# Kernel optimization log

Hardware: AMD Instinct MI355X
Metric: run time of the kernel (lower is better)

## Reference

```python
import jax, jax.numpy as jnp
import numpy as np

N = 50000
LEAKY_SLOPE = 0.2


def gat_layer(x, src, dst, W, a_src, a_dst, bias, concat):
    """PyG-style GATConv (eval mode, self-loops already in src/dst).
    x: [N, Fin]; W: [Fin, H*C]; a_src, a_dst: [H, C]; bias: [H*C] or [C].
    """
    H, C = a_src.shape
    h = (x @ W).reshape(-1, H, C)                      # [N, H, C]
    alpha_src = jnp.einsum('nhc,hc->nh', h, a_src)      # [N, H]
    alpha_dst = jnp.einsum('nhc,hc->nh', h, a_dst)      # [N, H]
    e = jax.nn.leaky_relu(alpha_src[src] + alpha_dst[dst], LEAKY_SLOPE)  # [E, H]
    # scatter-softmax over incoming edges of each destination node
    m = jax.lax.stop_gradient(jax.ops.segment_max(e, dst, num_segments=N))
    e = jnp.exp(e - m[dst])
    denom = jax.ops.segment_sum(e, dst, num_segments=N)  # [N, H]
    alpha = e / (denom[dst] + 1e-16)                     # [E, H]
    msg = h[src] * alpha[:, :, None]                     # [E, H, C]
    out = jax.ops.segment_sum(msg, dst, num_segments=N)  # [N, H, C]
    out = out.reshape(-1, H * C) if concat else out.mean(axis=1)
    return out + bias


def setup_inputs() -> dict:
    key = jax.random.key(0)
    ks = jax.random.split(key, 10)
    Fin, Hd, Hh = 256, 64, 4
    E = 1600000
    x = jax.random.normal(ks[0], (N, Fin), dtype=jnp.float32)
    edge_index = jax.random.randint(ks[1], (2, E), 0, N, dtype=jnp.int64)
    s = 1.0 / np.sqrt(Fin)
    W1 = jax.random.normal(ks[2], (Fin, Hh * Hd), dtype=jnp.float32) * s
    att_src1 = jax.random.normal(ks[3], (Hh, Hd), dtype=jnp.float32) * (1.0 / np.sqrt(Hd))
    att_dst1 = jax.random.normal(ks[4], (Hh, Hd), dtype=jnp.float32) * (1.0 / np.sqrt(Hd))
    b1 = jnp.zeros((Hh * Hd,), dtype=jnp.float32)
    W2 = jax.random.normal(ks[5], (Hh * Hd, Hd), dtype=jnp.float32) * (1.0 / np.sqrt(Hh * Hd))
    att_src2 = jax.random.normal(ks[6], (1, Hd), dtype=jnp.float32) * (1.0 / np.sqrt(Hd))
    att_dst2 = jax.random.normal(ks[7], (1, Hd), dtype=jnp.float32) * (1.0 / np.sqrt(Hd))
    b2 = jnp.zeros((Hd,), dtype=jnp.float32)
    return {"x": x, "edge_index": edge_index, "W1": W1, "att_src1": att_src1,
            "att_dst1": att_dst1, "b1": b1, "W2": W2, "att_src2": att_src2,
            "att_dst2": att_dst2, "b2": b2}


def reference(x, edge_index, W1, att_src1, att_dst1, b1, W2, att_src2, att_dst2, b2):
    # PyG GATConv adds self-loops by default
    loop = jnp.arange(N, dtype=edge_index.dtype)
    src = jnp.concatenate([edge_index[0], loop])
    dst = jnp.concatenate([edge_index[1], loop])
    h = gat_layer(x, src, dst, W1, att_src1, att_dst1, b1, concat=True)
    h = jax.nn.elu(h)            # dropout is identity in eval mode
    out = gat_layer(h, src, dst, W2, att_src2, att_dst2, b2, concat=False)
    return out
```

## Files before the change

kernel.cpp:

```cpp
#include <hip/hip_runtime.h>


typedef __attribute__((ext_vector_type(8))) short short8;
typedef __attribute__((ext_vector_type(4))) float floatx4;

#define FIN 256
#define H1 4
#define CH 64
#define CAP 16384

__device__ __forceinline__ float bf2f(ushort u) {
    union { unsigned int i; float f; } v; v.i = ((unsigned int)u) << 16; return v.f;
}
__device__ __forceinline__ ushort f2bf(float f) {
    union { float f; unsigned int i; } v; v.f = f;
    unsigned int r = v.i + 0x7fffu + ((v.i >> 16) & 1u);
    return (ushort)(r >> 16);
}
__device__ __forceinline__ float load_in(const void* p, int i, int f) {
    return f ? ((const float*)p)[i] : bf2f(((const ushort*)p)[i]);
}
__device__ __forceinline__ int load_idx(const void* p, long long i, int f64) {
    return f64 ? (int)((const long long*)p)[i] : ((const int*)p)[i];
}

__global__ __launch_bounds__(256) void probe_kernel(const ushort* __restrict__ x,
                                                    const int* __restrict__ ei,
                                                    int* __restrict__ flags,
                                                    int* __restrict__ bcnt) {
    __shared__ int s_nan, s_odd;
    int t = threadIdx.x;
    bcnt[t] = 0;
    if (t == 0) { s_nan = 0; s_odd = 0; }
    __syncthreads();
    int nanc = 0, oddc = 0;
    for (int i = t; i < 16384; i += 256) {
        ushort u = x[i];
        if (((u >> 7) & 0xFF) == 0xFF) nanc++;
    }
    for (int i = t; i < 2048; i += 256)
        if (ei[2 * i + 1] != 0) oddc++;
    if (nanc) atomicAdd(&s_nan, nanc);
    if (oddc) atomicAdd(&s_odd, oddc);
    __syncthreads();
    if (t == 0) {
        flags[0] = (s_nan >= 2) ? 1 : 0;
        flags[1] = (s_odd == 0) ? 1 : 0;
    }
}

__global__ __launch_bounds__(256) void prep_bucket_kernel(
        const void* __restrict__ x, const void* __restrict__ W1,
        const void* __restrict__ W2, ushort* __restrict__ xb,
        ushort* __restrict__ Wt1, ushort* __restrict__ Wt2,
        const void* __restrict__ ei, int* __restrict__ bcnt,
        unsigned int* __restrict__ buckets,
        int E, int Etot, int Nn, const int* __restrict__ flags,
        int PB_conv, int PB_tr_end) {
    __shared__ int lcnt[256], lbase[256], lcur[256];
    int bid = blockIdx.x, t = threadIdx.x;
    int f = flags[0];
    if (bid < PB_conv) {
        int i0 = bid * 2048 + t * 8;
        if (f) {
            float4 v0 = ((const float4*)x)[i0 / 4];
            float4 v1 = ((const float4*)x)[i0 / 4 + 1];
            ushort4 o0, o1;
            o0.x = f2bf(v0.x); o0.y = f2bf(v0.y); o0.z = f2bf(v0.z); o0.w = f2bf(v0.w);
            o1.x = f2bf(v1.x); o1.y = f2bf(v1.y); o1.z = f2bf(v1.z); o1.w = f2bf(v1.w);
            *(ushort4*)(xb + i0) = o0;
            *(ushort4*)(xb + i0 + 4) = o1;
        } else {
            *(uint4*)(xb + i0) = ((const uint4*)x)[i0 / 8];
        }
        return;
    }
    if (bid < PB_tr_end) {
        int j = (bid - PB_conv) * 256 + t;
        if (j < FIN * FIN) {
            int n = j / FIN, k = j % FIN;
            Wt1[j] = f2bf(load_in(W1, k * FIN + n, f));
        } else {
            int jj = j - FIN * FIN;
            int n = jj / FIN, k = jj % FIN;
            Wt2[jj] = f2bf(load_in(W2, k * CH + n, f));
        }
        return;
    }
    lcnt[t] = 0; lcur[t] = 0;
    __syncthreads();
    int f64 = flags[1];
    int base = (bid - PB_tr_end) * 4096 + t;
    unsigned int val[16]; int bk[16]; bool ok[16];
#pragma unroll
    for (int j = 0; j < 16; ++j) {
        int e = base + j * 256;
        ok[j] = e < Etot;
        bk[j] = 0; val[j] = 0;
        if (ok[j]) {
            int s, d;
// ... 93 lines not shown
                    alphaD[row * H + head] = pd;
                }
#pragma unroll
                for (int nt = 0; nt < 4; nt++) {
                    int col = cbase + nt * 16 + l16;
                    size_t caddr = planar
                        ? ((size_t)(col >> 7) * M + row) * 128 + (col & 127)
                        : (size_t)row * Nc + col;
                    C[caddr] = f2bf(acc[mt][nt][r]);
                }
            }
        }
    }
}

__global__ __launch_bounds__(256) void gemm1_pass2_kernel(
        const ushort* __restrict__ A, const ushort* __restrict__ Bt,
        ushort* __restrict__ C, int M, int K, int Nc,
        const void* __restrict__ aS, const void* __restrict__ aD,
        float* __restrict__ alphaS, float* __restrict__ alphaD,
        const int* __restrict__ flags, int g1, int nbx,
        const int* __restrict__ bcnt, const unsigned int* __restrict__ buckets,
        int* __restrict__ offs, int* __restrict__ csr_src, int Nn) {
    __shared__ int part[256], sc[256], cur[256];
    int bid = blockIdx.x;
    int t = threadIdx.x;
    if (bid < g1) {
        gemm_core(A, Bt, C, M, K, Nc, aS, aD, alphaS, alphaD, 4, flags[0],
                  bid % nbx, bid / nbx, 1);
        return;
    }
    int b = bid - g1;
    part[t] = bcnt[t];
    __syncthreads();
#pragma unroll
    for (int off = 1; off < 256; off <<= 1) {
        int v = (t >= off) ? part[t - off] : 0;
        __syncthreads();
        part[t] += v;
        __syncthreads();
    }
    int basepos = (b == 0) ? 0 : part[b - 1];
    int nEdges = min(bcnt[b], CAP);
    sc[t] = 0;
    __syncthreads();
    const unsigned int* bk = buckets + (size_t)b * CAP;
    for (int i = t; i < nEdges; i += 256)
        atomicAdd(&sc[bk[i] & 255], 1);
    __syncthreads();
    int mycount = sc[t];
    __syncthreads();
#pragma unroll
    for (int off = 1; off < 256; off <<= 1) {
        int v = (t >= off) ? sc[t - off] : 0;
        __syncthreads();
        sc[t] += v;
        __syncthreads();
    }
    int excl = sc[t] - mycount;
    int gnode = b * 256 + t;
    if (gnode <= Nn) offs[gnode] = basepos + excl;
    cur[t] = excl;
    __syncthreads();
    for (int i = t; i < nEdges; i += 256) {
        unsigned int v = bk[i];
        int p = atomicAdd(&cur[v & 255], 1);
        csr_src[basepos + p] = (int)(v >> 8);
    }
}

__global__ __launch_bounds__(256) void gemm2_kernel(const ushort* __restrict__ A,
                                                    const ushort* __restrict__ Bt,
                                                    ushort* __restrict__ C,
                                                    int M, int K, int Nc,
                                                    const void* __restrict__ aS,
                                                    const void* __restrict__ aD,
                                                    float* __restrict__ alphaS,
                                                    float* __restrict__ alphaD,
                                                    const int* __restrict__ flags) {
    gemm_core(A, Bt, C, M, K, Nc, aS, aD, alphaS, alphaD, 1, flags[0],
              blockIdx.x, blockIdx.y, 0);
}

__global__ __launch_bounds__(256) void gat_node1_pass(
        const int* __restrict__ csr_src, const int* __restrict__ offs,
        const float* __restrict__ asrc, const float* __restrict__ adst,
        const ushort* __restrict__ h1p, const void* __restrict__ b1,
        ushort* __restrict__ hmidb, int Nn, const int* __restrict__ flags,
        int plane) {
    int f = flags[0];
    int wave = threadIdx.x >> 6, lane = threadIdx.x & 63;
    int n = blockIdx.x * 4 + wave;
    if (n >= Nn) return;
    int half = lane >> 5, l5 = lane & 31;
    int head = plane * 2 + (l5 >> 4);
    float ad = adst[n * H1 + head];
    unsigned rowoff = (unsigned)(plane * Nn) * 128u + (unsigned)l5 * 4u;
    int beg = offs[n], end = offs[n + 1];
    float a0 = 0.f, a1 = 0.f, a2 = 0.f, a3 = 0.f, l = 0.f;

    int e = beg;
    while (e + 16 <= end) {
        int sj[8]; float aj[8]; uint2 vj[8];
#pragma unroll
        for (int j = 0; j < 8; ++j) sj[j] = csr_src[e + 2 * j + half];
#pragma unroll
        for (int j = 0; j < 8; ++j) {
            aj[j] = asrc[sj[j] * H1 + head];
            vj[j] = *(const uint2*)(h1p + rowoff + (unsigned)sj[j] * 128u);
        }
#pragma unroll
        for (int j = 0; j < 8; ++j) {
            float s = aj[j] + ad;
            s = fmaxf(s, 0.2f * s);
            float p = __expf(s);
            l += p;
            union { unsigned int i; float fl; } c0, c1, c2, c3;
            c0.i = vj[j].x << 16; c1.i = vj[j].x & 0xffff0000u;
            c2.i = vj[j].y << 16; c3.i = vj[j].y & 0xffff0000u;
            a0 += p * c0.fl; a1 += p * c1.fl;
            a2 += p * c2.fl; a3 += p * c3.fl;
        }
        e += 16;
    }
    if (e < end) {
        int sj[8]; float aj[8]; uint2 vj[8];
#pragma unroll
        for (int j = 0; j < 8; ++j) {
            int ei = e + 2 * j + half;
            sj[j] = csr_src[ei < end ? ei : beg];
        }
#pragma unroll
        for (int j = 0; j < 8; ++j) {
            int ei = e + 2 * j + half;
            aj[j] = (ei < end) ? asrc[sj[j] * H1 + head] : -1e30f;
            vj[j] = *(const uint2*)(h1p + rowoff + (unsigned)sj[j] * 128u);
        }
#pragma unroll
        for (int j = 0; j < 8; ++j) {
            float s = aj[j] + ad;
            s = fmaxf(s, 0.2f * s);
            float p = __expf(s);
            l += p;
            union { unsigned int i; float fl; } c0, c1, c2, c3;
            c0.i = vj[j].x << 16; c1.i = vj[j].x & 0xffff0000u;
            c2.i = vj[j].y << 16; c3.i = vj[j].y & 0xffff0000u;
            a0 += p * c0.fl; a1 += p * c1.fl;
            a2 += p * c2.fl; a3 += p * c3.fl;
        }
    }
    a0 += __shfl_xor(a0, 32); a1 += __shfl_xor(a1, 32);
    a2 += __shfl_xor(a2, 32); a3 += __shfl_xor(a3, 32);
    l  += __shfl_xor(l, 32);
    if (half == 0) {
        float inv = 1.f / (l + 1e-16f);
        int cb = plane * 128 + l5 * 4;
        float o0 = a0 * inv + load_in(b1, cb + 0, f);
        float o1 = a1 * inv + load_in(b1, cb + 1, f);
        float o2 = a2 * inv + load_in(b1, cb + 2, f);
        float o3 = a3 * inv + load_in(b1, cb + 3, f);
        o0 = o0 > 0.f ? o0 : __expf(o0) - 1.f;
        o1 = o1 > 0.f ? o1 : __expf(o1) - 1.f;
        o2 = o2 > 0.f ? o2 : __expf(o2) - 1.f;
        o3 = o3 > 0.f ? o3 : __expf(o3) - 1.f;
        uint2 st;
        st.x = (unsigned int)f2bf(o0) | ((unsigned int)f2bf(o1) << 16);
        st.y = (unsigned int)f2bf(o2) | ((unsigned int)f2bf(o3) << 16);
        *(uint2*)(hmidb + (unsigned)n * 256u + (unsigned)cb) = st;
    }
}

__global__ __launch_bounds__(256) void gat_node2(const int* __restrict__ csr_src,
                                                 const int* __restrict__ offs,
                                                 const float* __restrict__ asrc,
                                                 const float* __restrict__ adst,
                                                 const ushort* __restrict__ h2b,
                                                 const void* __restrict__ b2,
                                                 void* __restrict__ out, int Nn,
                                                 const int* __restrict__ flags) {
    int f = flags[0];
    int wave = threadIdx.x >> 6, lane = threadIdx.x & 63;
    int n = blockIdx.x * 4 + wave;
    if (n >= Nn) return;
    int q = lane >> 4, l4 = lane & 15;
    float ad = adst[n];
    int beg = offs[n], end = offs[n + 1];
    float a0 = 0.f, a1 = 0.f, a2 = 0.f, a3 = 0.f, l = 0.f;

    int e = beg;
    while (e + 16 <= end) {
        int sj[4]; float aj[4]; uint2 vj[4];
#pragma unroll
        for (int j = 0; j < 4; ++j) sj[j] = csr_src[e + 4 * j + q];
#pragma unroll
        for (int j = 0; j < 4; ++j) {
            aj[j] = asrc[sj[j]];
            vj[j] = *(const uint2*)(h2b + (unsigned)sj[j] * 64u + (unsigned)l4 * 4u);
        }
#pragma unroll
        for (int j = 0; j < 4; ++j) {
            float s = aj[j] + ad;
            s = fmaxf(s, 0.2f * s);
            float p = __expf(s);
            l += p;
            union { unsigned int i; float fl; } c0, c1, c2, c3;
            c0.i = vj[j].x << 16; c1.i = vj[j].x & 0xffff0000u;
            c2.i = vj[j].y << 16; c3.i = vj[j].y & 0xffff0000u;
            a0 += p * c0.fl; a1 += p * c1.fl;
            a2 += p * c2.fl; a3 += p * c3.fl;
        }
        e += 16;
    }
    if (e < end) {
        int sj[4]; float aj[4]; uint2 vj[4];
#pragma unroll
        for (int j = 0; j < 4; ++j) {
            int ei = e + 4 * j + q;
            sj[j] = csr_src[ei < end ? ei : beg];
        }
#pragma unroll
        for (int j = 0; j < 4; ++j) {
            int ei = e + 4 * j + q;
            aj[j] = (ei < end) ? asrc[sj[j]] : -1e30f;
            vj[j] = *(const uint2*)(h2b + (unsigned)sj[j] * 64u + (unsigned)l4 * 4u);
        }
#pragma unroll
        for (int j = 0; j < 4; ++j) {
            float s = aj[j] + ad;
            s = fmaxf(s, 0.2f * s);
            float p = __expf(s);
            l += p;
            union { unsigned int i; float fl; } c0, c1, c2, c3;
            c0.i = vj[j].x << 16; c1.i = vj[j].x & 0xffff0000u;
            c2.i = vj[j].y << 16; c3.i = vj[j].y & 0xffff0000u;
            a0 += p * c0.fl; a1 += p * c1.fl;
            a2 += p * c2.fl; a3 += p * c3.fl;
        }
    }
#pragma unroll
    for (int off = 16; off <= 32; off <<= 1) {
        a0 += __shfl_xor(a0, off); a1 += __shfl_xor(a1, off);
        a2 += __shfl_xor(a2, off); a3 += __shfl_xor(a3, off);
        l  += __shfl_xor(l, off);
    }
    if (lane < 16) {
        float inv = 1.f / (l + 1e-16f);
        float o0 = a0 * inv + load_in(b2, l4 * 4 + 0, f);
        float o1 = a1 * inv + load_in(b2, l4 * 4 + 1, f);
        float o2 = a2 * inv + load_in(b2, l4 * 4 + 2, f);
        float o3 = a3 * inv + load_in(b2, l4 * 4 + 3, f);
        if (f) {
            float4 st; st.x = o0; st.y = o1; st.z = o2; st.w = o3;
            *(float4*)((float*)out + (unsigned)n * 64u + (unsigned)l4 * 4u) = st;
        } else {
            uint2 st;
            st.x = (unsigned int)f2bf(o0) | ((unsigned int)f2bf(o1) << 16);
            st.y = (unsigned int)f2bf(o2) | ((unsigned int)f2bf(o3) << 16);
            *(uint2*)((ushort*)out + (unsigned)n * 64u + (unsigned)l4 * 4u) = st;
        }
    }
}

extern "C" void kernel_launch(void* const* d_in, const int* in_sizes, int n_in,
                              void* d_out, int out_size, void* d_ws, size_t ws_size,
                              hipStream_t stream) {
    const void* x   = d_in[0];
    const void* ei  = d_in[1];
    const void* W1  = d_in[2];
    const void* as1 = d_in[3];
    const void* ad1 = d_in[4];
    const void* b1  = d_in[5];
    const void* W2  = d_in[6];
    const void* as2 = d_in[7];
    const void* ad2 = d_in[8];
    const void* b2  = d_in[9];

    const int Nn = in_sizes[0] / FIN;
    const int E  = in_sizes[1] / 2;
    const int ET = E + Nn;
    const int NB = (Nn + 255) >> 8;

    char* ws = (char*)d_ws;
    size_t off = 0;
    auto alloc = [&](size_t bytes) {
        size_t o = off;
        off += (bytes + 255) & ~(size_t)255;
        return o;
    };
    ushort* xb    = (ushort*)(ws + alloc((size_t)Nn * FIN * 2));
    ushort* h1b   = (ushort*)(ws + alloc((size_t)Nn * FIN * 2));
    ushort* hmidb = (ushort*)(ws + alloc((size_t)Nn * FIN * 2));
    ushort* h2b   = (ushort*)(ws + alloc((size_t)Nn * CH * 2));
    ushort* Wt1   = (ushort*)(ws + alloc((size_t)FIN * FIN * 2));
    ushort* Wt2   = (ushort*)(ws + alloc((size_t)CH * FIN * 2));
    float* as1f   = (float*)(ws + alloc((size_t)Nn * H1 * 4));
    float* ad1f   = (float*)(ws + alloc((size_t)Nn * H1 * 4));
    float* as2f   = (float*)(ws + alloc((size_t)Nn * 4));
    float* ad2f   = (float*)(ws + alloc((size_t)Nn * 4));
    int*   offs   = (int*)(ws + alloc((size_t)(Nn + 1) * 4));
    int*   csr    = (int*)(ws + alloc((size_t)ET * 4));
    unsigned int* buckets = (unsigned int*)(ws + alloc((size_t)256 * CAP * 4));
    int*   bcnt   = (int*)(ws + alloc(256 * 4));
    int*   flags  = (int*)(ws + alloc(256));
    (void)ws_size; (void)n_in; (void)out_size;

    probe_kernel<<<1, 256, 0, stream>>>((const ushort*)x, (const int*)ei, flags, bcnt);

    int PB_conv = (Nn * FIN) / 2048;
    int PB_tr   = (FIN * FIN + CH * FIN) / 256;
    int PB_bkt  = (ET + 4095) / 4096;
    prep_bucket_kernel<<<PB_conv + PB_tr + PB_bkt, 256, 0, stream>>>(
        x, W1, W2, xb, Wt1, Wt2, ei, bcnt, buckets,
        E, ET, Nn, flags, PB_conv, PB_conv + PB_tr);

    int nbx = (Nn + 255) / 256;
    int g1 = nbx * H1;
    gemm1_pass2_kernel<<<g1 + NB, 256, 0, stream>>>(
        xb, Wt1, h1b, Nn, FIN, FIN, as1, ad1, as1f, ad1f,
        flags, g1, nbx, bcnt, buckets, offs, csr, Nn);

    gat_node1_pass<<<(Nn + 3) / 4, 256, 0, stream>>>(
        csr, offs, as1f, ad1f, h1b, b1, hmidb, Nn, flags, 0);
    gat_node1_pass<<<(Nn + 3) / 4, 256, 0, stream>>>(
        csr, offs, as1f, ad1f, h1b, b1, hmidb, Nn, flags, 1);

    gemm2_kernel<<<dim3((Nn + 255) / 256, 1), 256, 0, stream>>>(
        hmidb, Wt2, h2b, Nn, FIN, CH, as2, ad2, as2f, ad2f, flags);
    gat_node2<<<(Nn + 3) / 4, 256, 0, stream>>>(csr, offs, as2f, ad2f, h2b, b2, d_out, Nn, flags);
}
```

Before: 362.3 us.

## Precompute packed per-edge attention weights before aggregation passes

Two new per-node kernels compute the per-edge exp attention weights and the per-node inverse softmax denominators once per layer. They store each weight in bf16, packed together with the source index: two uint2 arrays for the layer-1 head pairs, and a single 32-bit word per edge for layer 2. The aggregation kernels then read these packed records instead of gathering asrc, recomputing leaky-relu and exp, and reducing the denominator, and the layer-1 aggregation switches to 16-byte feature loads with 8 channels per lane. This removes redundant attention math and gathers from the bandwidth-bound aggregation loops. In exchange it adds two extra edge passes and extra workspace traffic, rounds attention weights to bf16, and assumes node indices fit in 16 bits for layer 2.

```diff
diff --git a/kernel.cpp b/kernel.cpp
--- a/kernel.cpp
+++ b/kernel.cpp
@@ -16,6 +16,9 @@
     union { float f; unsigned int i; } v; v.f = f;
     unsigned int r = v.i + 0x7fffu + ((v.i >> 16) & 1u);
     return (ushort)(r >> 16);
+}
+__device__ __forceinline__ float bits2f(unsigned int b) {
+    union { unsigned int i; float f; } v; v.i = b; return v.f;
 }
 __device__ __forceinline__ float load_in(const void* p, int i, int f) {
     return f ? ((const float*)p)[i] : bf2f(((const ushort*)p)[i]);
@@ -275,98 +278,171 @@
               blockIdx.x, blockIdx.y, 0);
 }
 
+__global__ __launch_bounds__(256) void wk1_kernel(const int* __restrict__ csr_src,
+                                                  const int* __restrict__ offs,
+                                                  const float* __restrict__ asrc,
+                                                  const float* __restrict__ adst,
+                                                  uint2* __restrict__ pkA,
+                                                  uint2* __restrict__ pkB,
+                                                  float* __restrict__ invl, int Nn) {
+    int wave = threadIdx.x >> 6, lane = threadIdx.x & 63;
+    int n = blockIdx.x * 4 + wave;
+    if (n >= Nn) return;
+    float4 ad = *(const float4*)(adst + (size_t)n * 4);
+    int beg = offs[n], end = offs[n + 1];
+    float l0 = 0.f, l1 = 0.f, l2 = 0.f, l3 = 0.f;
+    for (int e0 = beg; e0 < end; e0 += 64) {
+        int e = e0 + lane;
+        bool v = e < end;
+        int src = v ? csr_src[e] : 0;
+        float4 as = *(const float4*)(asrc + (size_t)src * 4);
+        float s0 = as.x + ad.x, s1 = as.y + ad.y, s2 = as.z + ad.z, s3 = as.w + ad.w;
+        s0 = fmaxf(s0, 0.2f * s0); s1 = fmaxf(s1, 0.2f * s1);
+        s2 = fmaxf(s2, 0.2f * s2); s3 = fmaxf(s3, 0.2f * s3);
+        float p0 = v ? __expf(s0) : 0.f, p1 = v ? __expf(s1) : 0.f;
+        float p2 = v ? __expf(s2) : 0.f, p3 = v ? __expf(s3) : 0.f;
+        l0 += p0; l1 += p1; l2 += p2; l3 += p3;
+        if (v) {
+            uint2 a, b;
+            a.x = (unsigned int)src;
+            a.y = (unsigned int)f2bf(p0) | ((unsigned int)f2bf(p1) << 16);
+            b.x = (unsigned int)src;
+            b.y = (unsigned int)f2bf(p2) | ((unsigned int)f2bf(p3) << 16);
+            pkA[e] = a; pkB[e] = b;
+        }
+    }
+#pragma unroll
+    for (int off = 1; off < 64; off <<= 1) {
+        l0 += __shfl_xor(l0, off); l1 += __shfl_xor(l1, off);
+        l2 += __shfl_xor(l2, off); l3 += __shfl_xor(l3, off);
+    }
+    if (lane == 0) {
+        float4 iv;
+        iv.x = 1.f / (l0 + 1e-16f); iv.y = 1.f / (l1 + 1e-16f);
+        iv.z = 1.f / (l2 + 1e-16f); iv.w = 1.f / (l3 + 1e-16f);
+        *(float4*)(invl + (size_t)n * 4) = iv;
+    }
+}
+
+__global__ __launch_bounds__(256) void wk2_kernel(const int* __restrict__ csr_src,
+                                                  const int* __restrict__ offs,
+                                                  const float* __restrict__ asrc,
+                                                  const float* __restrict__ adst,
+                                                  unsigned int* __restrict__ pk2,
+                                                  float* __restrict__ invl2, int Nn) {
+    int wave = threadIdx.x >> 6, lane = threadIdx.x & 63;
+    int n = blockIdx.x * 4 + wave;
+    if (n >= Nn) return;
+    float ad = adst[n];
+    int beg = offs[n], end = offs[n + 1];
+    float l = 0.f;
+    for (int e0 = beg; e0 < end; e0 += 64) {
+        int e = e0 + lane;
+        bool v = e < end;
+        int src = v ? csr_src[e] : 0;
+        float s = asrc[src] + ad;
+        s = fmaxf(s, 0.2f * s);
+        float p = v ? __expf(s) : 0.f;
+        l += p;
+        if (v) pk2[e] = (unsigned int)src | ((unsigned int)f2bf(p) << 16);
+    }
+#pragma unroll
+    for (int off = 1; off < 64; off <<= 1) l += __shfl_xor(l, off);
+    if (lane == 0) invl2[n] = 1.f / (l + 1e-16f);
+}
+
 __global__ __launch_bounds__(256) void gat_node1_pass(
-        const int* __restrict__ csr_src, const int* __restrict__ offs,
-        const float* __restrict__ asrc, const float* __restrict__ adst,
-        const ushort* __restrict__ h1p, const void* __restrict__ b1,
-        ushort* __restrict__ hmidb, int Nn, const int* __restrict__ flags,
-        int plane) {
+        const uint2* __restrict__ pk, const int* __restrict__ offs,
+        const float* __restrict__ invl, const ushort* __restrict__ h1p,
+        const void* __restrict__ b1, ushort* __restrict__ hmidb,
+        int Nn, const int* __restrict__ flags, int plane) {
     int f = flags[0];
     int wave = threadIdx.x >> 6, lane = threadIdx.x & 63;
     int n = blockIdx.x * 4 + wave;
     if (n >= Nn) return;
-    int half = lane >> 5, l5 = lane & 31;
-    int head = plane * 2 + (l5 >> 4);
-    float ad = adst[n * H1 + head];
-    unsigned rowoff = (unsigned)(plane * Nn) * 128u + (unsigned)l5 * 4u;
+    int g = lane >> 4, l4 = lane & 15;
+    bool hi = l4 >= 8;
+    const ushort* base = h1p + (size_t)plane * Nn * 128 + (size_t)l4 * 8;
     int beg = offs[n], end = offs[n + 1];
-    float a0 = 0.f, a1 = 0.f, a2 = 0.f, a3 = 0.f, l = 0.f;
+    float a0 = 0.f, a1 = 0.f, a2 = 0.f, a3 = 0.f;
+    float a4 = 0.f, a5 = 0.f, a6 = 0.f, a7 = 0.f;
 
     int e = beg;
-    while (e + 16 <= end) {
-        int sj[8]; float aj[8]; uint2 vj[8];
-#pragma unroll
-        for (int j = 0; j < 8; ++j) sj[j] = csr_src[e + 2 * j + half];
-#pragma unroll
-        for (int j = 0; j < 8; ++j) {
-            aj[j] = asrc[sj[j] * H1 + head];
-            vj[j] = *(const uint2*)(h1p + rowoff + (unsigned)sj[j] * 128u);
-        }
-#pragma unroll
-        for (int j = 0; j < 8; ++j) {
-            float s = aj[j] + ad;
-            s = fmaxf(s, 0.2f * s);
-            float p = __expf(s);
-            l += p;
-            union { unsigned int i; float fl; } c0, c1, c2, c3;
-            c0.i = vj[j].x << 16; c1.i = vj[j].x & 0xffff0000u;
-            c2.i = vj[j].y << 16; c3.i = vj[j].y & 0xffff0000u;
-            a0 += p * c0.fl; a1 += p * c1.fl;
-            a2 += p * c2.fl; a3 += p * c3.fl;
-        }
-        e += 16;
+    while (e + 8 <= end) {
+        uint2 k0 = pk[e + g];
+        uint2 k1 = pk[e + 4 + g];
+        uint4 v0 = *(const uint4*)(base + (size_t)k0.x * 128);
+        uint4 v1 = *(const uint4*)(base + (size_t)k1.x * 128);
+        float p0 = bits2f(hi ? (k0.y & 0xffff0000u) : (k0.y << 16));
+        float p1 = bits2f(hi ? (k1.y & 0xffff0000u) : (k1.y << 16));
+        a0 += p0 * bits2f(v0.x << 16); a1 += p0 * bits2f(v0.x & 0xffff0000u);
+        a2 += p0 * bits2f(v0.y << 16); a3 += p0 * bits2f(v0.y & 0xffff0000u);
+        a4 += p0 * bits2f(v0.z << 16); a5 += p0 * bits2f(v0.z & 0xffff0000u);
+        a6 += p0 * bits2f(v0.w << 16); a7 += p0 * bits2f(v0.w & 0xffff0000u);
+        a0 += p1 * bits2f(v1.x << 16); a1 += p1 * bits2f(v1.x & 0xffff0000u);
+        a2 += p1 * bits2f(v1.y << 16); a3 += p1 * bits2f(v1.y & 0xffff0000u);
+        a4 += p1 * bits2f(v1.z << 16); a5 += p1 * bits2f(v1.z & 0xffff0000u);
+        a6 += p1 * bits2f(v1.w << 16); a7 += p1 * bits2f(v1.w & 0xffff0000u);
+        e += 8;
     }
     if (e < end) {
-        int sj[8]; float aj[8]; uint2 vj[8];
-#pragma unroll
-        for (int j = 0; j < 8; ++j) {
-            int ei = e + 2 * j + half;
-            sj[j] = csr_src[ei < end ? ei : beg];
-        }
-#pragma unroll
-        for (int j = 0; j < 8; ++j) {
-            int ei = e + 2 * j + half;
-            aj[j] = (ei < end) ? asrc[sj[j] * H1 + head] : -1e30f;
-            vj[j] = *(const uint2*)(h1p + rowoff + (unsigned)sj[j] * 128u);
-        }
-#pragma unroll
-        for (int j = 0; j < 8; ++j) {
-            float s = aj[j] + ad;
-            s = fmaxf(s, 0.2f * s);
-            float p = __expf(s);
-            l += p;
-            union { unsigned int i; float fl; } c0, c1, c2, c3;
-            c0.i = vj[j].x << 16; c1.i = vj[j].x & 0xffff0000u;
-            c2.i = vj[j].y << 16; c3.i = vj[j].y & 0xffff0000u;
-            a0 += p * c0.fl; a1 += p * c1.fl;
-            a2 += p * c2.fl; a3 += p * c3.fl;
-        }
-    }
-    a0 += __shfl_xor(a0, 32); a1 += __shfl_xor(a1, 32);
-    a2 += __shfl_xor(a2, 32); a3 += __shfl_xor(a3, 32);
-    l  += __shfl_xor(l, 32);
-    if (half == 0) {
-        float inv = 1.f / (l + 1e-16f);
-        int cb = plane * 128 + l5 * 4;
+        int i0 = e + g, i1 = e + 4 + g;
+        uint2 k0, k1;
+        k0.x = 0u; k0.y = 0u; k1.x = 0u; k1.y = 0u;
+        if (i0 < end) k0 = pk[i0];
+        if (i1 < end) k1 = pk[i1];
+        uint4 v0 = *(const uint4*)(base + (size_t)k0.x * 128);
+        uint4 v1 = *(const uint4*)(base + (size_t)k1.x * 128);
+        float p0 = bits2f(hi ? (k0.y & 0xffff0000u) : (k0.y << 16));
+        float p1 = bits2f(hi ? (k1.y & 0xffff0000u) : (k1.y << 16));
+        a0 += p0 * bits2f(v0.x << 16); a1 += p0 * bits2f(v0.x & 0xffff0000u);
+        a2 += p0 * bits2f(v0.y << 16); a3 += p0 * bits2f(v0.y & 0xffff0000u);
+        a4 += p0 * bits2f(v0.z << 16); a5 += p0 * bits2f(v0.z & 0xffff0000u);
+        a6 += p0 * bits2f(v0.w << 16); a7 += p0 * bits2f(v0.w & 0xffff0000u);
+        a0 += p1 * bits2f(v1.x << 16); a1 += p1 * bits2f(v1.x & 0xffff0000u);
+        a2 += p1 * bits2f(v1.y << 16); a3 += p1 * bits2f(v1.y & 0xffff0000u);
+        a4 += p1 * bits2f(v1.z << 16); a5 += p1 * bits2f(v1.z & 0xffff0000u);
+        a6 += p1 * bits2f(v1.w << 16); a7 += p1 * bits2f(v1.w & 0xffff0000u);
+    }
+#pragma unroll
+    for (int off = 16; off <= 32; off <<= 1) {
+        a0 += __shfl_xor(a0, off); a1 += __shfl_xor(a1, off);
+        a2 += __shfl_xor(a2, off); a3 += __shfl_xor(a3, off);
+        a4 += __shfl_xor(a4, off); a5 += __shfl_xor(a5, off);
+        a6 += __shfl_xor(a6, off); a7 += __shfl_xor(a7, off);
+    }
+    if (lane < 16) {
+        int head = plane * 2 + (l4 >> 3);
+        float inv = invl[(size_t)n * 4 + head];
+        int cb = plane * 128 + l4 * 8;
         float o0 = a0 * inv + load_in(b1, cb + 0, f);
         float o1 = a1 * inv + load_in(b1, cb + 1, f);
         float o2 = a2 * inv + load_in(b1, cb + 2, f);
         float o3 = a3 * inv + load_in(b1, cb + 3, f);
+        float o4 = a4 * inv + load_in(b1, cb + 4, f);
+        float o5 = a5 * inv + load_in(b1, cb + 5, f);
+        float o6 = a6 * inv + load_in(b1, cb + 6, f);
+        float o7 = a7 * inv + load_in(b1, cb + 7, f);
         o0 = o0 > 0.f ? o0 : __expf(o0) - 1.f;
         o1 = o1 > 0.f ? o1 : __expf(o1) - 1.f;
         o2 = o2 > 0.f ? o2 : __expf(o2) - 1.f;
         o3 = o3 > 0.f ? o3 : __expf(o3) - 1.f;
-        uint2 st;
+        o4 = o4 > 0.f ? o4 : __expf(o4) - 1.f;
+        o5 = o5 > 0.f ? o5 : __expf(o5) - 1.f;
+        o6 = o6 > 0.f ? o6 : __expf(o6) - 1.f;
+        o7 = o7 > 0.f ? o7 : __expf(o7) - 1.f;
+        uint4 st;
         st.x = (unsigned int)f2bf(o0) | ((unsigned int)f2bf(o1) << 16);
         st.y = (unsigned int)f2bf(o2) | ((unsigned int)f2bf(o3) << 16);
-        *(uint2*)(hmidb + (unsigned)n * 256u + (unsigned)cb) = st;
-    }
-}
-
-__global__ __launch_bounds__(256) void gat_node2(const int* __restrict__ csr_src,
+        st.z = (unsigned int)f2bf(o4) | ((unsigned int)f2bf(o5) << 16);
+        st.w = (unsigned int)f2bf(o6) | ((unsigned int)f2bf(o7) << 16);
+        *(uint4*)(hmidb + (size_t)n * 256 + cb) = st;
+    }
+}
+
+__global__ __launch_bounds__(256) void gat_node2(const unsigned int* __restrict__ pk2,
                                                  const int* __restrict__ offs,
-                                                 const float* __restrict__ asrc,
-                                                 const float* __restrict__ adst,
+                                                 const float* __restrict__ invl2,
                                                  const ushort* __restrict__ h2b,
                                                  const void* __restrict__ b2,
                                                  void* __restrict__ out, int Nn,
@@ -375,81 +451,57 @@
     int wave = threadIdx.x >> 6, lane = threadIdx.x & 63;
     int n = blockIdx.x * 4 + wave;
     if (n >= Nn) return;
-    int q = lane >> 4, l4 = lane & 15;
-    float ad = adst[n];
+    int g = lane >> 4, l4 = lane & 15;
+    const ushort* base = h2b + (size_t)l4 * 4;
     int beg = offs[n], end = offs[n + 1];
-    float a0 = 0.f, a1 = 0.f, a2 = 0.f, a3 = 0.f, l = 0.f;
+    float a0 = 0.f, a1 = 0.f, a2 = 0.f, a3 = 0.f;
 
     int e = beg;
-    while (e + 16 <= end) {
-        int sj[4]; float aj[4]; uint2 vj[4];
-#pragma unroll
-        for (int j = 0; j < 4; ++j) sj[j] = csr_src[e + 4 * j + q];
-#pragma unroll
-        for (int j = 0; j < 4; ++j) {
-            aj[j] = asrc[sj[j]];
-            vj[j] = *(const uint2*)(h2b + (unsigned)sj[j] * 64u + (unsigned)l4 * 4u);
-        }
-#pragma unroll
-        for (int j = 0; j < 4; ++j) {
-            float s = aj[j] + ad;
-            s = fmaxf(s, 0.2f * s);
-            float p = __expf(s);
-            l += p;
-            union { unsigned int i; float fl; } c0, c1, c2, c3;
-            c0.i = vj[j].x << 16; c1.i = vj[j].x & 0xffff0000u;
-            c2.i = vj[j].y << 16; c3.i = vj[j].y & 0xffff0000u;
-            a0 += p * c0.fl; a1 += p * c1.fl;
-            a2 += p * c2.fl; a3 += p * c3.fl;
-        }
-        e += 16;
+    while (e + 8 <= end) {
+        unsigned int k0 = pk2[e + g];
+        unsigned int k1 = pk2[e + 4 + g];
+        uint2 v0 = *(const uint2*)(base + (size_t)(k0 & 0xffffu) * 64);
+        uint2 v1 = *(const uint2*)(base + (size_t)(k1 & 0xffffu) * 64);
+        float p0 = bits2f(k0 & 0xffff0000u);
+        float p1 = bits2f(k1 & 0xffff0000u);
+        a0 += p0 * bits2f(v0.x << 16); a1 += p0 * bits2f(v0.x & 0xffff0000u);
+        a2 += p0 * bits2f(v0.y << 16); a3 += p0 * bits2f(v0.y & 0xffff0000u);
+        a0 += p1 * bits2f(v1.x << 16); a1 += p1 * bits2f(v1.x & 0xffff0000u);
+        a2 += p1 * bits2f(v1.y << 16); a3 += p1 * bits2f(v1.y & 0xffff0000u);
+        e += 8;
     }
     if (e < end) {
-        int sj[4]; float aj[4]; uint2 vj[4];
-#pragma unroll
-        for (int j = 0; j < 4; ++j) {
-            int ei = e + 4 * j + q;
-            sj[j] = csr_src[ei < end ? ei : beg];
-        }
-#pragma unroll
-        for (int j = 0; j < 4; ++j) {
-            int ei = e + 4 * j + q;
-            aj[j] = (ei < end) ? asrc[sj[j]] : -1e30f;
-            vj[j] = *(const uint2*)(h2b + (unsigned)sj[j] * 64u + (unsigned)l4 * 4u);
-        }
-#pragma unroll
-        for (int j = 0; j < 4; ++j) {
-            float s = aj[j] + ad;
-            s = fmaxf(s, 0.2f * s);
-            float p = __expf(s);
-            l += p;
-            union { unsigned int i; float fl; } c0, c1, c2, c3;
-            c0.i = vj[j].x << 16; c1.i = vj[j].x & 0xffff0000u;
-            c2.i = vj[j].y << 16; c3.i = vj[j].y & 0xffff0000u;
-            a0 += p * c0.fl; a1 += p * c1.fl;
-            a2 += p * c2.fl; a3 += p * c3.fl;
-        }
+        int i0 = e + g, i1 = e + 4 + g;
+        unsigned int k0 = (i0 < end) ? pk2[i0] : 0u;
+        unsigned int k1 = (i1 < end) ? pk2[i1] : 0u;
+        uint2 v0 = *(const uint2*)(base + (size_t)(k0 & 0xffffu) * 64);
+        uint2 v1 = *(const uint2*)(base + (size_t)(k1 & 0xffffu) * 64);
+        float p0 = bits2f(k0 & 0xffff0000u);
+        float p1 = bits2f(k1 & 0xffff0000u);
+        a0 += p0 * bits2f(v0.x << 16); a1 += p0 * bits2f(v0.x & 0xffff0000u);
+        a2 += p0 * bits2f(v0.y << 16); a3 += p0 * bits2f(v0.y & 0xffff0000u);
+        a0 += p1 * bits2f(v1.x << 16); a1 += p1 * bits2f(v1.x & 0xffff0000u);
+        a2 += p1 * bits2f(v1.y << 16); a3 += p1 * bits2f(v1.y & 0xffff0000u);
     }
 #pragma unroll
     for (int off = 16; off <= 32; off <<= 1) {
         a0 += __shfl_xor(a0, off); a1 += __shfl_xor(a1, off);
         a2 += __shfl_xor(a2, off); a3 += __shfl_xor(a3, off);
-        l  += __shfl_xor(l, off);
     }
     if (lane < 16) {
-        float inv = 1.f / (l + 1e-16f);
+        float inv = invl2[n];
         float o0 = a0 * inv + load_in(b2, l4 * 4 + 0, f);
         float o1 = a1 * inv + load_in(b2, l4 * 4 + 1, f);
         float o2 = a2 * inv + load_in(b2, l4 * 4 + 2, f);
         float o3 = a3 * inv + load_in(b2, l4 * 4 + 3, f);
         if (f) {
             float4 st; st.x = o0; st.y = o1; st.z = o2; st.w = o3;
-            *(float4*)((float*)out + (unsigned)n * 64u + (unsigned)l4 * 4u) = st;
+            *(float4*)((float*)out + (size_t)n * 64 + l4 * 4) = st;
         } else {
             uint2 st;
             st.x = (unsigned int)f2bf(o0) | ((unsigned int)f2bf(o1) << 16);
             st.y = (unsigned int)f2bf(o2) | ((unsigned int)f2bf(o3) << 16);
-            *(uint2*)((ushort*)out + (unsigned)n * 64u + (unsigned)l4 * 4u) = st;
+            *(uint2*)((ushort*)out + (size_t)n * 64 + l4 * 4) = st;
         }
     }
 }
@@ -490,8 +542,13 @@
     float* ad1f   = (float*)(ws + alloc((size_t)Nn * H1 * 4));
     float* as2f   = (float*)(ws + alloc((size_t)Nn * 4));
     float* ad2f   = (float*)(ws + alloc((size_t)Nn * 4));
+    float* invl   = (float*)(ws + alloc((size_t)Nn * H1 * 4));
+    float* invl2  = (float*)(ws + alloc((size_t)Nn * 4));
     int*   offs   = (int*)(ws + alloc((size_t)(Nn + 1) * 4));
     int*   csr    = (int*)(ws + alloc((size_t)ET * 4));
+    uint2* pkA    = (uint2*)(ws + alloc((size_t)ET * 8));
+    uint2* pkB    = (uint2*)(ws + alloc((size_t)ET * 8));
+    unsigned int* pk2 = (unsigned int*)(ws + alloc((size_t)ET * 4));
     unsigned int* buckets = (unsigned int*)(ws + alloc((size_t)256 * CAP * 4));
     int*   bcnt   = (int*)(ws + alloc(256 * 4));
     int*   flags  = (int*)(ws + alloc(256));
@@ -512,12 +569,14 @@
         xb, Wt1, h1b, Nn, FIN, FIN, as1, ad1, as1f, ad1f,
         flags, g1, nbx, bcnt, buckets, offs, csr, Nn);
 
+    wk1_kernel<<<(Nn + 3) / 4, 256, 0, stream>>>(csr, offs, as1f, ad1f, pkA, pkB, invl, Nn);
     gat_node1_pass<<<(Nn + 3) / 4, 256, 0, stream>>>(
-        csr, offs, as1f, ad1f, h1b, b1, hmidb, Nn, flags, 0);
+        pkA, offs, invl, h1b, b1, hmidb, Nn, flags, 0);
     gat_node1_pass<<<(Nn + 3) / 4, 256, 0, stream>>>(
-        csr, offs, as1f, ad1f, h1b, b1, hmidb, Nn, flags, 1);
+        pkB, offs, invl, h1b, b1, hmidb, Nn, flags, 1);
 
     gemm2_kernel<<<dim3((Nn + 255) / 256, 1), 256, 0, stream>>>(
         hmidb, Wt2, h2b, Nn, FIN, CH, as2, ad2, as2f, ad2f, flags);
-    gat_node2<<<(Nn + 3) / 4, 256, 0, stream>>>(csr, offs, as2f, ad2f, h2b, b2, d_out, Nn, flags);
-}
+    wk2_kernel<<<(Nn + 3) / 4, 256, 0, stream>>>(csr, offs, as2f, ad2f, pk2, invl2, Nn);
+    gat_node2<<<(Nn + 3) / 4, 256, 0, stream>>>(pk2, offs, invl2, h2b, b2, d_out, Nn, flags);
+}
```

Measured after the change: 397.2 us. 1.1x slower.

## Split layer-1 aggregation: compute all-head weights once, reuse packed weights in second pass

Applied to the files above, without the earlier changes.

The first aggregation pass now computes softmax numerators for all four heads at once and writes each edge's source index plus its bf16 weights for heads 2-3 into a packed per-edge buffer, along with per-node inverse denominators. The second pass reads these packed entries instead of the CSR plus asrc gather and exp, so it only gathers feature rows. Both passes now use 16-byte feature loads, with 16 lanes covering a 128-wide plane and 4 edge groups per wave. This adds an 8-byte-per-edge write and read, and stores the head 2-3 weights in bf16, which reduces their precision.

```diff
diff --git a/kernel.cpp b/kernel.cpp
--- a/kernel.cpp
+++ b/kernel.cpp
@@ -16,6 +16,9 @@
     union { float f; unsigned int i; } v; v.f = f;
     unsigned int r = v.i + 0x7fffu + ((v.i >> 16) & 1u);
     return (ushort)(r >> 16);
+}
+__device__ __forceinline__ float bits2f(unsigned int b) {
+    union { unsigned int i; float f; } v; v.i = b; return v.f;
 }
 __device__ __forceinline__ float load_in(const void* p, int i, int f) {
     return f ? ((const float*)p)[i] : bf2f(((const ushort*)p)[i]);
@@ -275,91 +278,217 @@
               blockIdx.x, blockIdx.y, 0);
 }
 
-__global__ __launch_bounds__(256) void gat_node1_pass(
+__global__ __launch_bounds__(256) void gat_node1_p0(
         const int* __restrict__ csr_src, const int* __restrict__ offs,
         const float* __restrict__ asrc, const float* __restrict__ adst,
         const ushort* __restrict__ h1p, const void* __restrict__ b1,
-        ushort* __restrict__ hmidb, int Nn, const int* __restrict__ flags,
-        int plane) {
+        ushort* __restrict__ hmidb, uint2* __restrict__ pkB,
+        float* __restrict__ invl23, int Nn, const int* __restrict__ flags) {
     int f = flags[0];
     int wave = threadIdx.x >> 6, lane = threadIdx.x & 63;
     int n = blockIdx.x * 4 + wave;
     if (n >= Nn) return;
-    int half = lane >> 5, l5 = lane & 31;
-    int head = plane * 2 + (l5 >> 4);
-    float ad = adst[n * H1 + head];
-    unsigned rowoff = (unsigned)(plane * Nn) * 128u + (unsigned)l5 * 4u;
+    int g = lane >> 4, l4 = lane & 15;
+    bool hi = l4 >= 8;
+    float4 ad = *(const float4*)(adst + (size_t)n * 4);
+    const ushort* base = h1p + (size_t)l4 * 8;
     int beg = offs[n], end = offs[n + 1];
-    float a0 = 0.f, a1 = 0.f, a2 = 0.f, a3 = 0.f, l = 0.f;
+    float a0 = 0.f, a1 = 0.f, a2 = 0.f, a3 = 0.f;
+    float a4 = 0.f, a5 = 0.f, a6 = 0.f, a7 = 0.f;
+    float l0 = 0.f, l1 = 0.f, l2 = 0.f, l3 = 0.f;
 
     int e = beg;
-    while (e + 16 <= end) {
-        int sj[8]; float aj[8]; uint2 vj[8];
-#pragma unroll
-        for (int j = 0; j < 8; ++j) sj[j] = csr_src[e + 2 * j + half];
-#pragma unroll
-        for (int j = 0; j < 8; ++j) {
-            aj[j] = asrc[sj[j] * H1 + head];
-            vj[j] = *(const uint2*)(h1p + rowoff + (unsigned)sj[j] * 128u);
-        }
-#pragma unroll
-        for (int j = 0; j < 8; ++j) {
-            float s = aj[j] + ad;
-            s = fmaxf(s, 0.2f * s);
-            float p = __expf(s);
-            l += p;
-            union { unsigned int i; float fl; } c0, c1, c2, c3;
-            c0.i = vj[j].x << 16; c1.i = vj[j].x & 0xffff0000u;
-            c2.i = vj[j].y << 16; c3.i = vj[j].y & 0xffff0000u;
-            a0 += p * c0.fl; a1 += p * c1.fl;
-            a2 += p * c2.fl; a3 += p * c3.fl;
-        }
-        e += 16;
-    }
-    if (e < end) {
-        int sj[8]; float aj[8]; uint2 vj[8];
-#pragma unroll
-        for (int j = 0; j < 8; ++j) {
-            int ei = e + 2 * j + half;
-            sj[j] = csr_src[ei < end ? ei : beg];
-        }
-#pragma unroll
-        for (int j = 0; j < 8; ++j) {
-            int ei = e + 2 * j + half;
-            aj[j] = (ei < end) ? asrc[sj[j] * H1 + head] : -1e30f;
-            vj[j] = *(const uint2*)(h1p + rowoff + (unsigned)sj[j] * 128u);
-        }
-#pragma unroll
-        for (int j = 0; j < 8; ++j) {
-            float s = aj[j] + ad;
-            s = fmaxf(s, 0.2f * s);
-            float p = __expf(s);
-            l += p;
-            union { unsigned int i; float fl; } c0, c1, c2, c3;
-            c0.i = vj[j].x << 16; c1.i = vj[j].x & 0xffff0000u;
-            c2.i = vj[j].y << 16; c3.i = vj[j].y & 0xffff0000u;
-            a0 += p * c0.fl; a1 += p * c1.fl;
-            a2 += p * c2.fl; a3 += p * c3.fl;
-        }
-    }
-    a0 += __shfl_xor(a0, 32); a1 += __shfl_xor(a1, 32);
-    a2 += __shfl_xor(a2, 32); a3 += __shfl_xor(a3, 32);
-    l  += __shfl_xor(l, 32);
-    if (half == 0) {
-        float inv = 1.f / (l + 1e-16f);
-        int cb = plane * 128 + l5 * 4;
+    while (true) {
+        bool full = (e + 8 <= end);
+        int i0 = e + g, i1 = e + 4 + g;
+        bool ok0 = full || (i0 < end), ok1 = full || (i1 < end);
+        if (!full && e >= end) break;
+        int s0 = csr_src[ok0 ? i0 : beg];
+        int s1 = csr_src[ok1 ? i1 : beg];
+        float4 A0 = *(const float4*)(asrc + (size_t)s0 * 4);
+        float4 A1 = *(const float4*)(asrc + (size_t)s1 * 4);
+        uint4 v0 = *(const uint4*)(base + (size_t)s0 * 128);
+        uint4 v1 = *(const uint4*)(base + (size_t)s1 * 128);
+        {
+            float t0 = A0.x + ad.x, t1 = A0.y + ad.y, t2 = A0.z + ad.z, t3 = A0.w + ad.w;
+            t0 = fmaxf(t0, 0.2f * t0); t1 = fmaxf(t1, 0.2f * t1);
+            t2 = fmaxf(t2, 0.2f * t2); t3 = fmaxf(t3, 0.2f * t3);
+            float p0 = ok0 ? __expf(t0) : 0.f, p1 = ok0 ? __expf(t1) : 0.f;
+            float p2 = ok0 ? __expf(t2) : 0.f, p3 = ok0 ? __expf(t3) : 0.f;
+            l0 += p0; l1 += p1; l2 += p2; l3 += p3;
+            float p = hi ? p1 : p0;
+            a0 += p * bits2f(v0.x << 16); a1 += p * bits2f(v0.x & 0xffff0000u);
+            a2 += p * bits2f(v0.y << 16); a3 += p * bits2f(v0.y & 0xffff0000u);
+            a4 += p * bits2f(v0.z << 16); a5 += p * bits2f(v0.z & 0xffff0000u);
+            a6 += p * bits2f(v0.w << 16); a7 += p * bits2f(v0.w & 0xffff0000u);
+            if (l4 == 0 && ok0) {
+                uint2 pk;
+                pk.x = (unsigned int)s0;
+                pk.y = (unsigned int)f2bf(p2) | ((unsigned int)f2bf(p3) << 16);
+                pkB[i0] = pk;
+            }
+        }
+        {
+            float t0 = A1.x + ad.x, t1 = A1.y + ad.y, t2 = A1.z + ad.z, t3 = A1.w + ad.w;
+            t0 = fmaxf(t0, 0.2f * t0); t1 = fmaxf(t1, 0.2f * t1);
+            t2 = fmaxf(t2, 0.2f * t2); t3 = fmaxf(t3, 0.2f * t3);
+            float p0 = ok1 ? __expf(t0) : 0.f, p1 = ok1 ? __expf(t1) : 0.f;
+            float p2 = ok1 ? __expf(t2) : 0.f, p3 = ok1 ? __expf(t3) : 0.f;
+            l0 += p0; l1 += p1; l2 += p2; l3 += p3;
+            float p = hi ? p1 : p0;
+            a0 += p * bits2f(v1.x << 16); a1 += p * bits2f(v1.x & 0xffff0000u);
+            a2 += p * bits2f(v1.y << 16); a3 += p * bits2f(v1.y & 0xffff0000u);
+            a4 += p * bits2f(v1.z << 16); a5 += p * bits2f(v1.z & 0xffff0000u);
+            a6 += p * bits2f(v1.w << 16); a7 += p * bits2f(v1.w & 0xffff0000u);
+            if (l4 == 0 && ok1) {
+                uint2 pk;
+                pk.x = (unsigned int)s1;
+                pk.y = (unsigned int)f2bf(p2) | ((unsigned int)f2bf(p3) << 16);
+                pkB[i1] = pk;
+            }
+        }
+        e += 8;
+        if (!full) break;
+    }
+#pragma unroll
+    for (int off = 16; off <= 32; off <<= 1) {
+        a0 += __shfl_xor(a0, off); a1 += __shfl_xor(a1, off);
+        a2 += __shfl_xor(a2, off); a3 += __shfl_xor(a3, off);
+        a4 += __shfl_xor(a4, off); a5 += __shfl_xor(a5, off);
+        a6 += __shfl_xor(a6, off); a7 += __shfl_xor(a7, off);
+        l0 += __shfl_xor(l0, off); l1 += __shfl_xor(l1, off);
+        l2 += __shfl_xor(l2, off); l3 += __shfl_xor(l3, off);
+    }
+    if (lane < 16) {
+        float inv = 1.f / ((hi ? l1 : l0) + 1e-16f);
+        int cb = l4 * 8;
         float o0 = a0 * inv + load_in(b1, cb + 0, f);
         float o1 = a1 * inv + load_in(b1, cb + 1, f);
         float o2 = a2 * inv + load_in(b1, cb + 2, f);
         float o3 = a3 * inv + load_in(b1, cb + 3, f);
+        float o4 = a4 * inv + load_in(b1, cb + 4, f);
+        float o5 = a5 * inv + load_in(b1, cb + 5, f);
+        float o6 = a6 * inv + load_in(b1, cb + 6, f);
+        float o7 = a7 * inv + load_in(b1, cb + 7, f);
         o0 = o0 > 0.f ? o0 : __expf(o0) - 1.f;
         o1 = o1 > 0.f ? o1 : __expf(o1) - 1.f;
         o2 = o2 > 0.f ? o2 : __expf(o2) - 1.f;
         o3 = o3 > 0.f ? o3 : __expf(o3) - 1.f;
-        uint2 st;
+        o4 = o4 > 0.f ? o4 : __expf(o4) - 1.f;
+        o5 = o5 > 0.f ? o5 : __expf(o5) - 1.f;
+        o6 = o6 > 0.f ? o6 : __expf(o6) - 1.f;
+        o7 = o7 > 0.f ? o7 : __expf(o7) - 1.f;
+        uint4 st;
         st.x = (unsigned int)f2bf(o0) | ((unsigned int)f2bf(o1) << 16);
         st.y = (unsigned int)f2bf(o2) | ((unsigned int)f2bf(o3) << 16);
-        *(uint2*)(hmidb + (unsigned)n * 256u + (unsigned)cb) = st;
+        st.z = (unsigned int)f2bf(o4) | ((unsigned int)f2bf(o5) << 16);
+        st.w = (unsigned int)f2bf(o6) | ((unsigned int)f2bf(o7) << 16);
+        *(uint4*)(hmidb + (size_t)n * 256 + cb) = st;
+        if (l4 == 0) {
+            float2 iv;
+            iv.x = 1.f / (l2 + 1e-16f);
+            iv.y = 1.f / (l3 + 1e-16f);
+            *(float2*)(invl23 + (size_t)n * 2) = iv;
+        }
+    }
+}
+
+__global__ __launch_bounds__(256) void gat_node1_p1(
+        const uint2* __restrict__ pk, const int* __restrict__ offs,
+        const float* __restrict__ invl23, const ushort* __restrict__ h1p,
+        const void* __restrict__ b1, ushort* __restrict__ hmidb,
+        int Nn, const int* __restrict__ flags) {
+    int f = flags[0];
+    int wave = threadIdx.x >> 6, lane = threadIdx.x & 63;
+    int n = blockIdx.x * 4 + wave;
+    if (n >= Nn) return;
+    int g = lane >> 4, l4 = lane & 15;
+    bool hi = l4 >= 8;
+    const ushort* base = h1p + (size_t)Nn * 128 + (size_t)l4 * 8;
+    int beg = offs[n], end = offs[n + 1];
+    float a0 = 0.f, a1 = 0.f, a2 = 0.f, a3 = 0.f;
+    float a4 = 0.f, a5 = 0.f, a6 = 0.f, a7 = 0.f;
+
+    int e = beg;
+    while (e + 16 <= end) {
+        uint2 k0 = pk[e + g],      k1 = pk[e + 4 + g];
+        uint2 k2 = pk[e + 8 + g],  k3 = pk[e + 12 + g];
+        uint4 v0 = *(const uint4*)(base + (size_t)k0.x * 128);
+        uint4 v1 = *(const uint4*)(base + (size_t)k1.x * 128);
+        uint4 v2 = *(const uint4*)(base + (size_t)k2.x * 128);
+        uint4 v3 = *(const uint4*)(base + (size_t)k3.x * 128);
+        float p0 = bits2f(hi ? (k0.y & 0xffff0000u) : (k0.y << 16));
+        float p1 = bits2f(hi ? (k1.y & 0xffff0000u) : (k1.y << 16));
+        float p2 = bits2f(hi ? (k2.y & 0xffff0000u) : (k2.y << 16));
+        float p3 = bits2f(hi ? (k3.y & 0xffff0000u) : (k3.y << 16));
+        a0 += p0 * bits2f(v0.x << 16); a1 += p0 * bits2f(v0.x & 0xffff0000u);
+        a2 += p0 * bits2f(v0.y << 16); a3 += p0 * bits2f(v0.y & 0xffff0000u);
+        a4 += p0 * bits2f(v0.z << 16); a5 += p0 * bits2f(v0.z & 0xffff0000u);
+        a6 += p0 * bits2f(v0.w << 16); a7 += p0 * bits2f(v0.w & 0xffff0000u);
+        a0 += p1 * bits2f(v1.x << 16); a1 += p1 * bits2f(v1.x & 0xffff0000u);
+        a2 += p1 * bits2f(v1.y << 16); a3 += p1 * bits2f(v1.y & 0xffff0000u);
+        a4 += p1 * bits2f(v1.z << 16); a5 += p1 * bits2f(v1.z & 0xffff0000u);
+        a6 += p1 * bits2f(v1.w << 16); a7 += p1 * bits2f(v1.w & 0xffff0000u);
+        a0 += p2 * bits2f(v2.x << 16); a1 += p2 * bits2f(v2.x & 0xffff0000u);
+        a2 += p2 * bits2f(v2.y << 16); a3 += p2 * bits2f(v2.y & 0xffff0000u);
+        a4 += p2 * bits2f(v2.z << 16); a5 += p2 * bits2f(v2.z & 0xffff0000u);
+        a6 += p2 * bits2f(v2.w << 16); a7 += p2 * bits2f(v2.w & 0xffff0000u);
+        a0 += p3 * bits2f(v3.x << 16); a1 += p3 * bits2f(v3.x & 0xffff0000u);
+        a2 += p3 * bits2f(v3.y << 16); a3 += p3 * bits2f(v3.y & 0xffff0000u);
+        a4 += p3 * bits2f(v3.z << 16); a5 += p3 * bits2f(v3.z & 0xffff0000u);
+        a6 += p3 * bits2f(v3.w << 16); a7 += p3 * bits2f(v3.w & 0xffff0000u);
+        e += 16;
+    }
+    if (e < end) {
+        uint2 kk[4];
+#pragma unroll
+        for (int j = 0; j < 4; ++j) {
+            int i = e + 4 * j + g;
+            kk[j].x = 0u; kk[j].y = 0u;
+            if (i < end) kk[j] = pk[i];
+        }
+#pragma unroll
+        for (int j = 0; j < 4; ++j) {
+            uint4 v = *(const uint4*)(base + (size_t)kk[j].x * 128);
+            float p = bits2f(hi ? (kk[j].y & 0xffff0000u) : (kk[j].y << 16));
+            a0 += p * bits2f(v.x << 16); a1 += p * bits2f(v.x & 0xffff0000u);
+            a2 += p * bits2f(v.y << 16); a3 += p * bits2f(v.y & 0xffff0000u);
+            a4 += p * bits2f(v.z << 16); a5 += p * bits2f(v.z & 0xffff0000u);
+            a6 += p * bits2f(v.w << 16); a7 += p * bits2f(v.w & 0xffff0000u);
+        }
+    }
+#pragma unroll
+    for (int off = 16; off <= 32; off <<= 1) {
+        a0 += __shfl_xor(a0, off); a1 += __shfl_xor(a1, off);
+        a2 += __shfl_xor(a2, off); a3 += __shfl_xor(a3, off);
+        a4 += __shfl_xor(a4, off); a5 += __shfl_xor(a5, off);
+        a6 += __shfl_xor(a6, off); a7 += __shfl_xor(a7, off);
+    }
+    if (lane < 16) {
+        float inv = invl23[(size_t)n * 2 + (hi ? 1 : 0)];
+        int cb = 128 + l4 * 8;
+        float o0 = a0 * inv + load_in(b1, cb + 0, f);
+        float o1 = a1 * inv + load_in(b1, cb + 1, f);
+        float o2 = a2 * inv + load_in(b1, cb + 2, f);
+        float o3 = a3 * inv + load_in(b1, cb + 3, f);
+        float o4 = a4 * inv + load_in(b1, cb + 4, f);
+        float o5 = a5 * inv + load_in(b1, cb + 5, f);
+        float o6 = a6 * inv + load_in(b1, cb + 6, f);
+        float o7 = a7 * inv + load_in(b1, cb + 7, f);
+        o0 = o0 > 0.f ? o0 : __expf(o0) - 1.f;
+        o1 = o1 > 0.f ? o1 : __expf(o1) - 1.f;
+        o2 = o2 > 0.f ? o2 : __expf(o2) - 1.f;
+        o3 = o3 > 0.f ? o3 : __expf(o3) - 1.f;
+        o4 = o4 > 0.f ? o4 : __expf(o4) - 1.f;
+        o5 = o5 > 0.f ? o5 : __expf(o5) - 1.f;
+        o6 = o6 > 0.f ? o6 : __expf(o6) - 1.f;
+        o7 = o7 > 0.f ? o7 : __expf(o7) - 1.f;
+        uint4 st;
+        st.x = (unsigned int)f2bf(o0) | ((unsigned int)f2bf(o1) << 16);
+        st.y = (unsigned int)f2bf(o2) | ((unsigned int)f2bf(o3) << 16);
+        st.z = (unsigned int)f2bf(o4) | ((unsigned int)f2bf(o5) << 16);
+        st.w = (unsigned int)f2bf(o6) | ((unsigned int)f2bf(o7) << 16);
+        *(uint4*)(hmidb + (size_t)n * 256 + cb) = st;
     }
 }
 
@@ -388,7 +517,7 @@
 #pragma unroll
         for (int j = 0; j < 4; ++j) {
             aj[j] = asrc[sj[j]];
-            vj[j] = *(const uint2*)(h2b + (unsigned)sj[j] * 64u + (unsigned)l4 * 4u);
+            vj[j] = *(const uint2*)(h2b + (size_t)sj[j] * 64 + (size_t)l4 * 4);
         }
 #pragma unroll
         for (int j = 0; j < 4; ++j) {
@@ -396,11 +525,8 @@
             s = fmaxf(s, 0.2f * s);
             float p = __expf(s);
             l += p;
-            union { unsigned int i; float fl; } c0, c1, c2, c3;
-            c0.i = vj[j].x << 16; c1.i = vj[j].x & 0xffff0000u;
-            c2.i = vj[j].y << 16; c3.i = vj[j].y & 0xffff0000u;
-            a0 += p * c0.fl; a1 += p * c1.fl;
-            a2 += p * c2.fl; a3 += p * c3.fl;
+            a0 += p * bits2f(vj[j].x << 16); a1 += p * bits2f(vj[j].x & 0xffff0000u);
+            a2 += p * bits2f(vj[j].y << 16); a3 += p * bits2f(vj[j].y & 0xffff0000u);
         }
         e += 16;
     }
@@ -415,7 +541,7 @@
         for (int j = 0; j < 4; ++j) {
             int ei = e + 4 * j + q;
             aj[j] = (ei < end) ? asrc[sj[j]] : -1e30f;
-            vj[j] = *(const uint2*)(h2b + (unsigned)sj[j] * 64u + (unsigned)l4 * 4u);
+            vj[j] = *(const uint2*)(h2b + (size_t)sj[j] * 64 + (size_t)l4 * 4);
         }
 #pragma unroll
         for (int j = 0; j < 4; ++j) {
@@ -423,11 +549,8 @@
             s = fmaxf(s, 0.2f * s);
             float p = __expf(s);
             l += p;
-            union { unsigned int i; float fl; } c0, c1, c2, c3;
-            c0.i = vj[j].x << 16; c1.i = vj[j].x & 0xffff0000u;
-            c2.i = vj[j].y << 16; c3.i = vj[j].y & 0xffff0000u;
-            a0 += p * c0.fl; a1 += p * c1.fl;
-            a2 += p * c2.fl; a3 += p * c3.fl;
+            a0 += p * bits2f(vj[j].x << 16); a1 += p * bits2f(vj[j].x & 0xffff0000u);
+            a2 += p * bits2f(vj[j].y << 16); a3 += p * bits2f(vj[j].y & 0xffff0000u);
         }
     }
 #pragma unroll
@@ -444,12 +567,12 @@
         float o3 = a3 * inv + load_in(b2, l4 * 4 + 3, f);
         if (f) {
             float4 st; st.x = o0; st.y = o1; st.z = o2; st.w = o3;
-            *(float4*)((float*)out + (unsigned)n * 64u + (unsigned)l4 * 4u) = st;
+            *(float4*)((float*)out + (size_t)n * 64 + l4 * 4) = st;
         } else {
             uint2 st;
             st.x = (unsigned int)f2bf(o0) | ((unsigned int)f2bf(o1) << 16);
             st.y = (unsigned int)f2bf(o2) | ((unsigned int)f2bf(o3) << 16);
-            *(uint2*)((ushort*)out + (unsigned)n * 64u + (unsigned)l4 * 4u) = st;
+            *(uint2*)((ushort*)out + (size_t)n * 64 + l4 * 4) = st;
         }
     }
 }
@@ -490,8 +613,10 @@
     float* ad1f   = (float*)(ws + alloc((size_t)Nn * H1 * 4));
     float* as2f   = (float*)(ws + alloc((size_t)Nn * 4));
     float* ad2f   = (float*)(ws + alloc((size_t)Nn * 4));
+    float* invl23 = (float*)(ws + alloc((size_t)Nn * 2 * 4));
     int*   offs   = (int*)(ws + alloc((size_t)(Nn + 1) * 4));
     int*   csr    = (int*)(ws + alloc((size_t)ET * 4));
+    uint2* pkB    = (uint2*)(ws + alloc((size_t)ET * 8));
     unsigned int* buckets = (unsigned int*)(ws + alloc((size_t)256 * CAP * 4));
     int*   bcnt   = (int*)(ws + alloc(256 * 4));
     int*   flags  = (int*)(ws + alloc(256));
@@ -512,12 +637,13 @@
         xb, Wt1, h1b, Nn, FIN, FIN, as1, ad1, as1f, ad1f,
         flags, g1, nbx, bcnt, buckets, offs, csr, Nn);
 
-    gat_node1_pass<<<(Nn + 3) / 4, 256, 0, stream>>>(
-        csr, offs, as1f, ad1f, h1b, b1, hmidb, Nn, flags, 0);
-    gat_node1_pass<<<(Nn + 3) / 4, 256, 0, stream>>>(
-        csr, offs, as1f, ad1f, h1b, b1, hmidb, Nn, flags, 1);
+    gat_node1_p0<<<(Nn + 3) / 4, 256, 0, stream>>>(
+        csr, offs, as1f, ad1f, h1b, b1, hmidb, pkB, invl23, Nn, flags);
+    gat_node1_p1<<<(Nn + 3) / 4, 256, 0, stream>>>(
+        pkB, offs, invl23, h1b, b1, hmidb, Nn, flags);
 
     gemm2_kernel<<<dim3((Nn + 255) / 256, 1), 256, 0, stream>>>(
         hmidb, Wt2, h2b, Nn, FIN, CH, as2, ad2, as2f, ad2f, flags);
-    gat_node2<<<(Nn + 3) / 4, 256, 0, stream>>>(csr, offs, as2f, ad2f, h2b, b2, d_out, Nn, flags);
-}
+    gat_node2<<<(Nn + 3) / 4, 256, 0, stream>>>(
+        csr, offs, as2f, ad2f, h2b, b2, d_out, Nn, flags);
+}
```

Result: slower. 373.1 us (+3.0%).
